# Kernel optimization log

Hardware: AMD Instinct MI355X
Metric: run time of the kernel (lower is better)

## Reference

```python
import jax, jax.numpy as jnp
import numpy as np

NUM_GROUPS = 32
EPS = 1e-6


def group_norm(x, gamma, beta):
    b, c, h, w = x.shape
    xg = x.reshape(b, NUM_GROUPS, c // NUM_GROUPS, h, w)
    mean = jnp.mean(xg, axis=(2, 3, 4), keepdims=True)
    var = jnp.var(xg, axis=(2, 3, 4), keepdims=True)
    xg = (xg - mean) * jax.lax.rsqrt(var + EPS)
    x = xg.reshape(b, c, h, w)
    return x * gamma[None, :, None, None] + beta[None, :, None, None]


def conv1x1(x, w, b):
    # x: [B,C,H,W], w: [Cout,Cin], b: [Cout]
    return jnp.einsum('bchw,oc->bohw', x, w) + b[None, :, None, None]


def setup_inputs() -> dict:
    key = jax.random.key(0)
    ks = jax.random.split(key, 11)
    B, C, H, W = 2, 512, 64, 64
    s = 1.0 / np.sqrt(C)
    return {
        'x': jax.random.normal(ks[0], (B, C, H, W), jnp.float32),
        'norm_gamma': jnp.ones((C,), jnp.float32),
        'norm_beta': jnp.zeros((C,), jnp.float32),
        'wq': jax.random.normal(ks[1], (C, C), jnp.float32) * s,
        'bq': jnp.zeros((C,), jnp.float32),
        'wk': jax.random.normal(ks[2], (C, C), jnp.float32) * s,
        'bk': jnp.zeros((C,), jnp.float32),
        'wv': jax.random.normal(ks[3], (C, C), jnp.float32) * s,
        'bv': jnp.zeros((C,), jnp.float32),
        'wo': jax.random.normal(ks[4], (C, C), jnp.float32) * s,
        'bo': jnp.zeros((C,), jnp.float32),
    }


def reference(x, norm_gamma, norm_beta, wq, bq, wk, bk, wv, bv, wo, bo):
    b, c, h, w = x.shape
    hn = group_norm(x, norm_gamma, norm_beta)
    q = conv1x1(hn, wq, bq).reshape(b, c, h * w)  # [B,C,HW]
    k = conv1x1(hn, wk, bk).reshape(b, c, h * w)
    v = conv1x1(hn, wv, bv).reshape(b, c, h * w)
    scale = jnp.asarray(c, x.dtype) ** -0.5
    # scores[b,i,j] = sum_c q[b,c,i] * k[b,c,j]
    scores = jnp.einsum('bci,bcj->bij', q, k) * scale
    attn = jax.nn.softmax(scores, axis=2)
    # out[b,c,i] = sum_j v[b,c,j] * attn[b,i,j]
    out = jnp.einsum('bcj,bij->bci', v, attn).reshape(b, c, h, w)
    out = conv1x1(out, wo, bo)
    return x + out
```

## Files before the change

### kernel.cpp

```cpp
#include <hip/hip_runtime.h>
#include <hip/hip_bf16.h>

using u16 = unsigned short;
typedef __attribute__((ext_vector_type(4))) float f32x4;
typedef __attribute__((ext_vector_type(8))) __bf16 bf16x8;
typedef __attribute__((ext_vector_type(8))) short s16x8;
typedef __attribute__((ext_vector_type(4))) short s16x4;

#define DEVI __device__ __forceinline__

constexpr int BATCH = 2, C = 512, HW = 4096, NG = 32, CPG = 16;

DEVI float b2f(u16 u) { union { unsigned u; float f; } a; a.u = ((unsigned)u) << 16; return a.f; }
DEVI u16 f2b(float f) {
  union { float f; unsigned u; } a; a.f = f;
  unsigned r = a.u + 0x7fffu + ((a.u >> 16) & 1u);
  return (u16)(r >> 16);
}

DEVI void xcd_remap(int& bx, int& by, int& bz) {
  const int nx = gridDim.x, ny = gridDim.y;
  const int nwg = nx * ny * gridDim.z;
  const int flat = blockIdx.x + nx * (blockIdx.y + ny * blockIdx.z);
  const int cpx = nwg >> 3;
  const int w = (flat & 7) * cpx + (flat >> 3);
  bx = w % nx;
  const int t = w / nx;
  by = t % ny;
  bz = t / ny;
}

__global__ __launch_bounds__(256) void cvt_w(const float* __restrict__ a, const float* __restrict__ b,
                                             const float* __restrict__ c, const float* __restrict__ d,
                                             u16* __restrict__ out) {
  int i = blockIdx.x * 256 + threadIdx.x;
  int w = i >> 16;
  int off = (i & 65535) * 4;
  const float* s = (w == 0) ? a : (w == 1) ? b : (w == 2) ? c : d;
  f32x4 v = *(const f32x4*)(s + off);
  s16x4 o;
  o[0] = (short)f2b(v[0]); o[1] = (short)f2b(v[1]); o[2] = (short)f2b(v[2]); o[3] = (short)f2b(v[3]);
  *(s16x4*)(out + (size_t)w * 262144 + off) = o;
}

__global__ __launch_bounds__(1024) void gn_stats(const float* __restrict__ x, float* __restrict__ stats) {
  int bg = blockIdx.x;
  const f32x4* xg = (const f32x4*)(x + (size_t)bg * (CPG * HW));
  float s = 0.f, ss = 0.f;
  for (int i = threadIdx.x; i < CPG * HW / 4; i += 1024) {
    f32x4 v = xg[i];
    s += v[0] + v[1] + v[2] + v[3];
    ss += v[0] * v[0] + v[1] * v[1] + v[2] * v[2] + v[3] * v[3];
  }
  #pragma unroll
  for (int o = 32; o; o >>= 1) { s += __shfl_xor(s, o); ss += __shfl_xor(ss, o); }
  __shared__ float red[32];
  int wv = threadIdx.x >> 6, ln = threadIdx.x & 63;
  if (ln == 0) { red[wv] = s; red[16 + wv] = ss; }
  __syncthreads();
  if (threadIdx.x == 0) {
    float S = 0.f, SS = 0.f;
    for (int i = 0; i < 16; ++i) { S += red[i]; SS += red[16 + i]; }
    float inv = 1.f / (float)(CPG * HW);
    float mean = S * inv;
    float var = SS * inv - mean * mean;
    stats[bg * 2] = mean;
    stats[bg * 2 + 1] = rsqrtf(var + 1e-6f);
  }
}

__global__ __launch_bounds__(256) void gn_normT(const float* __restrict__ x, const float* __restrict__ stats,
                                                const float* __restrict__ gamma, const float* __restrict__ beta,
                                                u16* __restrict__ hnT) {
  __shared__ u16 tile[64][66];
  int b = blockIdx.z, c0 = blockIdx.y * 64, h0 = blockIdx.x * 64;
  int t = threadIdx.x;
  const float* xb = x + ((size_t)b * C + c0) * HW + h0;
  int r = t / 16, cc = (t % 16) * 4;
  #pragma unroll
  for (int it = 0; it < 4; ++it) {
    int rr = it * 16 + r;
    int ch = c0 + rr;
    int g = b * NG + (ch >> 4);
    float mean = stats[g * 2], rstd = stats[g * 2 + 1];
    float ga = gamma[ch] * rstd;
    float be = beta[ch] - mean * ga;
    f32x4 v = *(const f32x4*)(xb + (size_t)rr * HW + cc);
    #pragma unroll
    for (int j = 0; j < 4; ++j) tile[rr][cc + j] = f2b(v[j] * ga + be);
  }
  __syncthreads();
  u16* op = hnT + (size_t)b * HW * C + (size_t)h0 * C + c0;
  int hr2 = t / 8, cg = (t % 8) * 8;
  #pragma unroll
  for (int it = 0; it < 2; ++it) {
    int hr = it * 32 + hr2;
    s16x8 o8;
    #pragma unroll
    for (int j = 0; j < 8; ++j) o8[j] = (short)tile[cg + j][hr];
    *(s16x8*)(op + (size_t)hr * C + cg) = o8;
  }
}

#define EPI_BIAS_M 1
#define EPI_BIAS_N 2
#define EPI_RESID  4
#define EPI_F32OUT 8
#define EPI_QK     32

template <int EPI>
__global__ __launch_bounds__(256) void gemm_bt(const u16* __restrict__ A, const u16* __restrict__ Bt,
                                               void* __restrict__ Co, int M, int N, int K,
                                               long long sA, long long sB, long long sC,
                                               const float* __restrict__ bias,
                                               const float* __restrict__ biasB,
                                               const float* __restrict__ resid, long long sR) {
  (void)M;
  __shared__ u16 ldsA[128 * 64];
  __shared__ u16 ldsB[128 * 64];
  const int tid = threadIdx.x;
  int bn, bm, bz;
  xcd_remap(bn, bm, bz);
  A += (size_t)bz * sA;
  Bt += (size_t)bz * sB;
  const int wave = tid >> 6, lane = tid & 63;
  const int wr = wave >> 1, wc = wave & 1;
  f32x4 acc[4][4] = {};

  const int srow = tid >> 3;
  const int sch = (tid & 7) ^ (srow & 7);
  const u16* gA = A + (size_t)(bm * 128 + srow) * K + sch * 8;
  const u16* gB = Bt + (size_t)(bn * 128 + srow) * K + sch * 8;
  u16* lA = ldsA + wave * 512;
  u16* lB = ldsB + wave * 512;

  for (int k0 = 0; k0 < K; k0 += 64) {
    #pragma unroll
    for (int cc = 0; cc < 4; ++cc) {
      __builtin_amdgcn_global_load_lds(
          (const __attribute__((address_space(1))) void*)(gA + (size_t)cc * 32 * K + k0),
          (__attribute__((address_space(3))) void*)(lA + cc * 2048), 16, 0, 0);
      __builtin_amdgcn_global_load_lds(
          (const __attribute__((address_space(1))) void*)(gB + (size_t)cc * 32 * K + k0),
          (__attribute__((address_space(3))) void*)(lB + cc * 2048), 16, 0, 0);
    }
    __syncthreads();
    #pragma unroll
    for (int kk = 0; kk < 2; ++kk) {
      bf16x8 af[4], bfv[4];
      #pragma unroll
      for (int m = 0; m < 4; ++m) {
        int r = wr * 64 + m * 16 + (lane & 15);
        int chunk = (kk * 4 + (lane >> 4)) ^ (r & 7);
        af[m] = *(const bf16x8*)(ldsA + r * 64 + chunk * 8);
      }
      #pragma unroll
      for (int n = 0; n < 4; ++n) {
        int r = wc * 64 + n * 16 + (lane & 15);
        int chunk = (kk * 4 + (lane >> 4)) ^ (r & 7);
        bfv[n] = *(const bf16x8*)(ldsB + r * 64 + chunk * 8);
      }
      #pragma unroll
      for (int m = 0; m < 4; ++m)
        #pragma unroll
        for (int n = 0; n < 4; ++n)
          acc[m][n] = __builtin_amdgcn_mfma_f32_16x16x32_bf16(af[m], bfv[n], acc[m][n], 0, 0, 0);
    }
    __syncthreads();
  }

  const int col0 = bn * 128 + wc * 64;
  const int row0 = bm * 128 + wr * 64 + ((lane >> 4) << 2);
  #pragma unroll
  for (int m = 0; m < 4; ++m) {
    #pragma unroll
    for (int j = 0; j < 4; ++j) {
      int gm = row0 + m * 16 + j;
      float bm_v = (EPI & EPI_BIAS_M) ? bias[gm] : 0.f;
      #pragma unroll
      for (int n = 0; n < 4; ++n) {
        int gn = col0 + n * 16 + (lane & 15);
        float v = acc[m][n][j] + bm_v;
        if (EPI & EPI_BIAS_N) {
          if (EPI & EPI_QK) v += (gn < 512) ? bias[gn] : biasB[gn - 512];
          else v += bias[gn];
        }
        if (EPI & EPI_RESID) v += resid[(size_t)bz * sR + (size_t)gm * N + gn];
        if (EPI & EPI_F32OUT)
          ((float*)Co)[(size_t)bz * sC + (size_t)gm * N + gn] = v;
        else
          ((u16*)Co)[(size_t)bz * sC + (size_t)gm * N + gn] = f2b(v);
      }
    }
  }
}

template <bool SCALED>
__global__ __launch_bounds__(512, 2) void gemm256(
    const u16* __restrict__ Ag, const u16* __restrict__ Bg,
    u16* __restrict__ Co, u16* __restrict__ Co2, int zSwitch,
    int Nld, int ldK, int nsplitLog, int kLen,
    long long sA, long long sB, long long sC, float scale) {
  __shared__ u16 lds[65536];
  const int tid = threadIdx.x;
  const int lane = tid & 63, w = tid >> 6;
  const int wm = w >> 2, wn = w & 3;
  const int l15 = lane & 15, l4 = lane >> 4;
  int bn, bm, z;
  xcd_remap(bn, bm, z);
  const int bz = z >> nsplitLog, kz = z & ((1 << nsplitLog) - 1);
  const int kStart = kz * kLen;
  const int NT = kLen >> 6;

  const int rStage = w * 8 + (lane >> 3);
  const int gch = (lane & 7) ^ (lane >> 3);
  const u16* gA = Ag + (size_t)bz * sA + (size_t)(bm * 256) * ldK + kStart + gch * 8;
  const u16* gB = Bg + (size_t)bz * sB + (size_t)(bn * 256) * ldK + kStart + gch * 8;

  f32x4 acc[8][4] = {};
  bf16x8 aF[4][2], bF[2][2][2];

  const int hB = wn >> 1, qB = wn & 1;
  const u16* pA0 = lds + (0 * 4 + wm) * 8192;
  const u16* pA1 = lds + (1 * 4 + wm) * 8192;
  const u16* pB0 = lds + (0 * 4 + 2 + hB) * 8192;
  const u16* pB1 = lds + (1 * 4 + 2 + hB) * 8192;

  #define STAGE(TT, DB, AB, HF) { \
    const u16* gbase = (AB) ? gB : gA; \
    u16* l0 = lds + ((DB) * 4 + (AB) * 2 + (HF)) * 8192 + w * 512; \
    _Pragma("unroll") for (int s = 0; s < 2; ++s) { \
      const u16* gp = gbase + (size_t)((HF) * 128 + s * 64 + rStage) * ldK + (TT) * 64; \
      __builtin_amdgcn_global_load_lds((const __attribute__((address_space(1))) void*)gp, \
          (__attribute__((address_space(3))) void*)(l0 + s * 4096), 16, 0, 0); } }

  #define LOAD_A(P, MH) { _Pragma("unroll") for (int j = 0; j < 4; ++j) \
    _Pragma("unroll") for (int kk = 0; kk < 2; ++kk) { \
      const int r_ = (MH) * 64 + j * 16 + l15; const int c_ = (kk * 4 + l4) ^ (r_ & 7); \
      aF[j][kk] = *(const bf16x8*)((P) + r_ * 64 + c_ * 8); } }

  #define LOAD_B(P, NH) { _Pragma("unroll") for (int j = 0; j < 2; ++j) \
    _Pragma("unroll") for (int kk = 0; kk < 2; ++kk) { \
      const int r_ = qB * 64 + (NH) * 32 + j * 16 + l15; const int c_ = (kk * 4 + l4) ^ (r_ & 7); \
      bF[NH][j][kk] = *(const bf16x8*)((P) + r_ * 64 + c_ * 8); } }

  #define MM(MH, NH) { __builtin_amdgcn_s_setprio(1); \
    _Pragma("unroll") for (int j = 0; j < 4; ++j) \
      _Pragma("unroll") for (int j2 = 0; j2 < 2; ++j2) \
        _Pragma("unroll") for (int kk = 0; kk < 2; ++kk) \
          acc[(MH) * 4 + j][(NH) * 2 + j2] = __builtin_amdgcn_mfma_f32_16x16x32_bf16( \
              aF[j][kk], bF[NH][j2][kk], acc[(MH) * 4 + j][(NH) * 2 + j2], 0, 0, 0); \
    __builtin_amdgcn_s_setprio(0); }

  #define BAR __builtin_amdgcn_s_barrier()
  #define WLG { asm volatile("s_waitcnt lgkmcnt(0)" ::: "memory"); __builtin_amdgcn_sched_barrier(0); }
  #define WV4 asm volatile("s_waitcnt vmcnt(4)" ::: "memory")
  #define WV0 asm volatile("s_waitcnt vmcnt(0)" ::: "memory")

  STAGE(0, 0, 1, 0); STAGE(0, 0, 1, 1);
  STAGE(0, 0, 0, 0); STAGE(0, 0, 0, 1);
  STAGE(1, 1, 1, 0); STAGE(1, 1, 1, 1);
  WV4; BAR;

  const int NI = NT / 2 - 1;
  for (int i = 0; i < NI; ++i) {
    const int t1 = 2 * i + 1, u0 = 2 * i + 2, u1 = 2 * i + 3;
    LOAD_A(pA0, 0); LOAD_B(pB0, 0); STAGE(t1, 1, 0, 0); BAR; WLG; MM(0, 0); BAR;
    LOAD_B(pB0, 1); STAGE(t1, 1, 0, 1); BAR; WLG; MM(0, 1); BAR;
    LOAD_A(pA0, 1); STAGE(u0, 0, 1, 0); BAR; WLG; MM(1, 1); BAR;
    STAGE(u0, 0, 1, 1); BAR; WLG; MM(1, 0); WV4; BAR;
    LOAD_A(pA1, 0); LOAD_B(pB1, 0); STAGE(u0, 0, 0, 0); BAR; WLG; MM(0, 0); BAR;
    LOAD_B(pB1, 1); STAGE(u0, 0, 0, 1); BAR; WLG; MM(0, 1); BAR;
    LOAD_A(pA1, 1); STAGE(u1, 1, 1, 0); BAR; WLG; MM(1, 1); BAR;
    STAGE(u1, 1, 1, 1); BAR; WLG; MM(1, 0); WV4; BAR;
  }
  {
    const int t1 = NT - 1;
    LOAD_A(pA0, 0); LOAD_B(pB0, 0); STAGE(t1, 1, 0, 0); BAR; WLG; MM(0, 0); BAR;
    LOAD_B(pB0, 1); STAGE(t1, 1, 0, 1); BAR; WLG; MM(0, 1); BAR;
    LOAD_A(pA0, 1); BAR; WLG; MM(1, 1); BAR;
    BAR; WLG; MM(1, 0); WV0; BAR;
    LOAD_A(pA1, 0); LOAD_B(pB1, 0); BAR; WLG; MM(0, 0); BAR;
    LOAD_B(pB1, 1); BAR; WLG; MM(0, 1); BAR;
    LOAD_A(pA1, 1); BAR; WLG; MM(1, 1); BAR;
    MM(1, 0);
  }
  #undef STAGE
  #undef LOAD_A
  #undef LOAD_B
  #undef MM
  #undef BAR
  #undef WLG
  #undef WV4
  #undef WV0

  {
    const int rloc = wm * 128 + l4 * 4;
    const int cloc = wn * 64 + l15;
    #pragma unroll
    for (int m = 0; m < 8; ++m) {
      #pragma unroll
      for (int j = 0; j < 4; ++j) {
        const int r_ = rloc + m * 16 + j;
        const int xr = ((r_ >> 2) & 3) << 5;
        #pragma unroll
        for (int n = 0; n < 4; ++n) {
          float v = acc[m][n][j];
          if (SCALED) v *= scale;
          *(u16*)((char*)lds + ((r_ * 512 + (cloc + n * 16) * 2) ^ xr)) = f2b(v);
        }
      }
    }
    __syncthreads();
    u16* outp = (z < zSwitch) ? (Co + (size_t)z * sC) : (Co2 + (size_t)(z - zSwitch) * sC);
    #pragma unroll
    for (int it = 0; it < 16; ++it) {
      const int idx = it * 512 + tid;
      const int r_ = idx >> 5, ch = idx & 31;
      const int xr = ((r_ >> 2) & 3) << 5;
      s16x8 d8 = *(const s16x8*)((const char*)lds + ((r_ * 512 + ch * 16) ^ xr));
      *(s16x8*)(outp + (size_t)(bm * 256 + r_) * Nld + bn * 256 + ch * 8) = d8;
    }
  }
}

__global__ __launch_bounds__(256) void softmax_rows(u16* __restrict__ S) {
  int row = blockIdx.x * 4 + (threadIdx.x >> 6);
  int lane = threadIdx.x & 63;
  s16x8* p = (s16x8*)(S + (size_t)row * 4096);
  float v[64];
  float m = -1e30f;
  #pragma unroll
  for (int j = 0; j < 8; ++j) {
    s16x8 raw = p[j * 64 + lane];
    #pragma unroll
    for (int e = 0; e < 8; ++e) {
      float f = b2f((u16)raw[e]);
      v[j * 8 + e] = f;
      m = fmaxf(m, f);
    }
  }
  #pragma unroll
  for (int o = 32; o; o >>= 1) m = fmaxf(m, __shfl_xor(m, o));
  float s = 0.f;
  #pragma unroll
  for (int i = 0; i < 64; ++i) { v[i] = __expf(v[i] - m); s += v[i]; }
  #pragma unroll
  for (int o = 32; o; o >>= 1) s += __shfl_xor(s, o);
  float r = 1.f / s;
  #pragma unroll
  for (int j = 0; j < 8; ++j) {
    s16x8 o8;
    #pragma unroll
    for (int e = 0; e < 8; ++e) o8[e] = (short)f2b(v[j * 8 + e] * r);
    p[j * 64 + lane] = o8;
  }
}

__global__ __launch_bounds__(256) void reduce_pv(const u16* __restrict__ P, const u16* __restrict__ P2,
                                                 u16* __restrict__ ao) {
  const size_t e = ((size_t)blockIdx.x * 256 + threadIdx.x) * 8;
  const int b = (int)(e >> 21);
  const size_t o = e & 2097151;
  float s[8] = {0.f, 0.f, 0.f, 0.f, 0.f, 0.f, 0.f, 0.f};
  #pragma unroll
  for (int kz = 0; kz < 4; ++kz) {
    const int zz = b * 4 + kz;
    const u16* src = (zz < 6) ? (P + (size_t)zz * 2097152) : (P2 + (size_t)(zz - 6) * 2097152);
    s16x8 v = *(const s16x8*)(src + o);
    #pragma unroll
    for (int j = 0; j < 8; ++j) s[j] += b2f((u16)v[j]);
  }
  s16x8 o8;
  #pragma unroll
  for (int j = 0; j < 8; ++j) o8[j] = (short)f2b(s[j]);
  *(s16x8*)(ao + e) = o8;
}

extern "C" void kernel_launch(void* const* d_in, const int* in_sizes, int n_in,
                              void* d_out, int out_size, void* d_ws, size_t ws_size,
                              hipStream_t stream) {
  (void)in_sizes; (void)n_in; (void)out_size; (void)ws_size;
  const float* x     = (const float*)d_in[0];
  const float* gamma = (const float*)d_in[1];
  const float* beta  = (const float*)d_in[2];
  const float* wq    = (const float*)d_in[3];
  const float* bq    = (const float*)d_in[4];
  const float* wk    = (const float*)d_in[5];
  const float* bk    = (const float*)d_in[6];
  const float* wv    = (const float*)d_in[7];
  const float* bv    = (const float*)d_in[8];
  const float* wo    = (const float*)d_in[9];
  const float* bo    = (const float*)d_in[10];

  char* ws = (char*)d_ws;
  const size_t MiB = 1024 * 1024;
  float* stats = (float*)ws;
  u16* wbf = (u16*)(ws + 1024);
  u16* vv  = (u16*)(ws + 4 * MiB);
  u16* qkT = (u16*)(ws + 12 * MiB);
  u16* hnT = (u16*)(ws + 28 * MiB);
  u16* Ppart = (u16*)(ws + 12 * MiB);
  u16* Sm  = (u16*)(ws + 36 * MiB);
  u16* aoT = (u16*)(ws + 36 * MiB);

  const long long sTok  = (long long)HW * C;
  const long long sTok2 = (long long)HW * 1024;
  const long long sS    = (long long)HW * HW;
  const float scale = 0.044194173824159216f;

  cvt_w<<<dim3(1024), dim3(256), 0, stream>>>(wq, wk, wv, wo, wbf);
  gn_stats<<<dim3(64), dim3(1024), 0, stream>>>(x, stats);
  gn_normT<<<dim3(HW / 64, C / 64, BATCH), dim3(256), 0, stream>>>(x, stats, gamma, beta, hnT);

  gemm_bt<EPI_BIAS_N | EPI_QK><<<dim3(8, 32, BATCH), dim3(256), 0, stream>>>(
      hnT, wbf, qkT, HW, 1024, C, sTok, 0, sTok2, bq, bk, nullptr, 0);
  gemm_bt<EPI_BIAS_M><<<dim3(32, 4, BATCH), dim3(256), 0, stream>>>(
      wbf + 2 * 262144, hnT, vv, C, HW, C, 0, sTok, sTok, bv, nullptr, nullptr, 0);

  gemm256<true><<<dim3(16, 16, BATCH), dim3(512), 0, stream>>>(
      qkT, qkT + 512, Sm, Sm, 1000, HW, 1024, 0, C, sTok2, sTok2, sS, scale);

  softmax_rows<<<dim3(2048), dim3(256), 0, stream>>>(Sm);

  gemm256<false><<<dim3(2, 16, BATCH * 4), dim3(512), 0, stream>>>(
      Sm, vv, Ppart, (u16*)d_out, 6, C, HW, 2, HW / 4, sS, sTok, (long long)2097152, 1.f);

  reduce_pv<<<dim3(2048), dim3(256), 0, stream>>>(Ppart, (const u16*)d_out, aoT);

  gemm_bt<EPI_BIAS_M | EPI_RESID | EPI_F32OUT><<<dim3(32, 4, BATCH), dim3(256), 0, stream>>>(
      wbf + 3 * 262144, aoT, d_out, C, HW, C, 0, sTok, (long long)C * HW, bo, nullptr, x, (long long)C * HW);
}
```

Before: 178.9 us.

## Add simple double-buffered schedule variant for PV GEMM and drop explicit lgkm waits

```diff
diff --git a/kernel.cpp b/kernel.cpp
--- a/kernel.cpp
+++ b/kernel.cpp
@@ -195,7 +195,7 @@
   }
 }
 
-template <bool SCALED>
+template <bool SCALED, int SCHED>
 __global__ __launch_bounds__(512, 2) void gemm256(
     const u16* __restrict__ Ag, const u16* __restrict__ Bg,
     u16* __restrict__ Co, u16* __restrict__ Co2, int zSwitch,
@@ -219,6 +219,7 @@
 
   f32x4 acc[8][4] = {};
   bf16x8 aF[4][2], bF[2][2][2];
+  bf16x8 aFB[8][2], bFB[4][2];
 
   const int hB = wn >> 1, qB = wn & 1;
   const u16* pA0 = lds + (0 * 4 + wm) * 8192;
@@ -252,48 +253,82 @@
               aF[j][kk], bF[NH][j2][kk], acc[(MH) * 4 + j][(NH) * 2 + j2], 0, 0, 0); \
     __builtin_amdgcn_s_setprio(0); }
 
+  #define READ_ALL(PA, PB) { \
+    _Pragma("unroll") for (int m = 0; m < 8; ++m) \
+      _Pragma("unroll") for (int kk = 0; kk < 2; ++kk) { \
+        const int r_ = m * 16 + l15; const int c_ = (kk * 4 + l4) ^ (r_ & 7); \
+        aFB[m][kk] = *(const bf16x8*)((PA) + r_ * 64 + c_ * 8); } \
+    _Pragma("unroll") for (int n = 0; n < 4; ++n) \
+      _Pragma("unroll") for (int kk = 0; kk < 2; ++kk) { \
+        const int r_ = qB * 64 + n * 16 + l15; const int c_ = (kk * 4 + l4) ^ (r_ & 7); \
+        bFB[n][kk] = *(const bf16x8*)((PB) + r_ * 64 + c_ * 8); } }
+
+  #define MM_ALL { __builtin_amdgcn_s_setprio(1); \
+    _Pragma("unroll") for (int m = 0; m < 8; ++m) \
+      _Pragma("unroll") for (int n = 0; n < 4; ++n) \
+        _Pragma("unroll") for (int kk = 0; kk < 2; ++kk) \
+          acc[m][n] = __builtin_amdgcn_mfma_f32_16x16x32_bf16( \
+              aFB[m][kk], bFB[n][kk], acc[m][n], 0, 0, 0); \
+    __builtin_amdgcn_s_setprio(0); }
+
   #define BAR __builtin_amdgcn_s_barrier()
-  #define WLG { asm volatile("s_waitcnt lgkmcnt(0)" ::: "memory"); __builtin_amdgcn_sched_barrier(0); }
   #define WV4 asm volatile("s_waitcnt vmcnt(4)" ::: "memory")
   #define WV0 asm volatile("s_waitcnt vmcnt(0)" ::: "memory")
 
-  STAGE(0, 0, 1, 0); STAGE(0, 0, 1, 1);
-  STAGE(0, 0, 0, 0); STAGE(0, 0, 0, 1);
-  STAGE(1, 1, 1, 0); STAGE(1, 1, 1, 1);
-  WV4; BAR;
-
-  const int NI = NT / 2 - 1;
-  for (int i = 0; i < NI; ++i) {
-    const int t1 = 2 * i + 1, u0 = 2 * i + 2, u1 = 2 * i + 3;
-    LOAD_A(pA0, 0); LOAD_B(pB0, 0); STAGE(t1, 1, 0, 0); BAR; WLG; MM(0, 0); BAR;
-    LOAD_B(pB0, 1); STAGE(t1, 1, 0, 1); BAR; WLG; MM(0, 1); BAR;
-    LOAD_A(pA0, 1); STAGE(u0, 0, 1, 0); BAR; WLG; MM(1, 1); BAR;
-    STAGE(u0, 0, 1, 1); BAR; WLG; MM(1, 0); WV4; BAR;
-    LOAD_A(pA1, 0); LOAD_B(pB1, 0); STAGE(u0, 0, 0, 0); BAR; WLG; MM(0, 0); BAR;
-    LOAD_B(pB1, 1); STAGE(u0, 0, 0, 1); BAR; WLG; MM(0, 1); BAR;
-    LOAD_A(pA1, 1); STAGE(u1, 1, 1, 0); BAR; WLG; MM(1, 1); BAR;
-    STAGE(u1, 1, 1, 1); BAR; WLG; MM(1, 0); WV4; BAR;
-  }
-  {
-    const int t1 = NT - 1;
-    LOAD_A(pA0, 0); LOAD_B(pB0, 0); STAGE(t1, 1, 0, 0); BAR; WLG; MM(0, 0); BAR;
-    LOAD_B(pB0, 1); STAGE(t1, 1, 0, 1); BAR; WLG; MM(0, 1); BAR;
-    LOAD_A(pA0, 1); BAR; WLG; MM(1, 1); BAR;
-    BAR; WLG; MM(1, 0); WV0; BAR;
-    LOAD_A(pA1, 0); LOAD_B(pB1, 0); BAR; WLG; MM(0, 0); BAR;
-    LOAD_B(pB1, 1); BAR; WLG; MM(0, 1); BAR;
-    LOAD_A(pA1, 1); BAR; WLG; MM(1, 1); BAR;
-    MM(1, 0);
+  if constexpr (SCHED == 0) {
+    STAGE(0, 0, 1, 0); STAGE(0, 0, 1, 1);
+    STAGE(0, 0, 0, 0); STAGE(0, 0, 0, 1);
+    STAGE(1, 1, 1, 0); STAGE(1, 1, 1, 1);
+    WV4; BAR;
+
+    const int NI = NT / 2 - 1;
+    for (int i = 0; i < NI; ++i) {
+      const int t1 = 2 * i + 1, u0 = 2 * i + 2, u1 = 2 * i + 3;
+      LOAD_A(pA0, 0); LOAD_B(pB0, 0); STAGE(t1, 1, 0, 0); BAR; MM(0, 0); BAR;
+      LOAD_B(pB0, 1); STAGE(t1, 1, 0, 1); BAR; MM(0, 1); BAR;
+      LOAD_A(pA0, 1); STAGE(u0, 0, 1, 0); BAR; MM(1, 1); BAR;
+      STAGE(u0, 0, 1, 1); BAR; MM(1, 0); WV4; BAR;
+      LOAD_A(pA1, 0); LOAD_B(pB1, 0); STAGE(u0, 0, 0, 0); BAR; MM(0, 0); BAR;
+      LOAD_B(pB1, 1); STAGE(u0, 0, 0, 1); BAR; MM(0, 1); BAR;
+      LOAD_A(pA1, 1); STAGE(u1, 1, 1, 0); BAR; MM(1, 1); BAR;
+      STAGE(u1, 1, 1, 1); BAR; MM(1, 0); WV4; BAR;
+    }
+    {
+      const int t1 = NT - 1;
+      LOAD_A(pA0, 0); LOAD_B(pB0, 0); STAGE(t1, 1, 0, 0); BAR; MM(0, 0); BAR;
+      LOAD_B(pB0, 1); STAGE(t1, 1, 0, 1); BAR; MM(0, 1); BAR;
+      LOAD_A(pA0, 1); BAR; MM(1, 1); BAR;
+      BAR; MM(1, 0); WV0; BAR;
+      LOAD_A(pA1, 0); LOAD_B(pB1, 0); BAR; MM(0, 0); BAR;
+      LOAD_B(pB1, 1); BAR; MM(0, 1); BAR;
+      LOAD_A(pA1, 1); BAR; MM(1, 1); BAR;
+      MM(1, 0);
+    }
+  } else {
+    STAGE(0, 0, 0, 0); STAGE(0, 0, 0, 1); STAGE(0, 0, 1, 0); STAGE(0, 0, 1, 1);
+    WV0; BAR;
+    for (int t = 0; t < NT; t += 2) {
+      if (t + 1 < NT) { STAGE(t + 1, 1, 0, 0); STAGE(t + 1, 1, 0, 1); STAGE(t + 1, 1, 1, 0); STAGE(t + 1, 1, 1, 1); }
+      READ_ALL(pA0, pB0);
+      MM_ALL;
+      WV0; BAR;
+      if (t + 2 < NT) { STAGE(t + 2, 0, 0, 0); STAGE(t + 2, 0, 0, 1); STAGE(t + 2, 0, 1, 0); STAGE(t + 2, 0, 1, 1); }
+      READ_ALL(pA1, pB1);
+      MM_ALL;
+      WV0; BAR;
+    }
   }
   #undef STAGE
   #undef LOAD_A
   #undef LOAD_B
   #undef MM
+  #undef READ_ALL
+  #undef MM_ALL
   #undef BAR
-  #undef WLG
   #undef WV4
   #undef WV0
 
+  __syncthreads();
   {
     const int rloc = wm * 128 + l4 * 4;
     const int cloc = wn * 64 + l15;
@@ -418,12 +453,12 @@
   gemm_bt<EPI_BIAS_M><<<dim3(32, 4, BATCH), dim3(256), 0, stream>>>(
       wbf + 2 * 262144, hnT, vv, C, HW, C, 0, sTok, sTok, bv, nullptr, nullptr, 0);
 
-  gemm256<true><<<dim3(16, 16, BATCH), dim3(512), 0, stream>>>(
+  gemm256<true, 0><<<dim3(16, 16, BATCH), dim3(512), 0, stream>>>(
       qkT, qkT + 512, Sm, Sm, 1000, HW, 1024, 0, C, sTok2, sTok2, sS, scale);
 
   softmax_rows<<<dim3(2048), dim3(256), 0, stream>>>(Sm);
 
-  gemm256<false><<<dim3(2, 16, BATCH * 4), dim3(512), 0, stream>>>(
+  gemm256<false, 1><<<dim3(2, 16, BATCH * 4), dim3(512), 0, stream>>>(
       Sm, vv, Ppart, (u16*)d_out, 6, C, HW, 2, HW / 4, sS, sTok, (long long)2097152, 1.f);
 
   reduce_pv<<<dim3(2048), dim3(256), 0, stream>>>(Ppart, (const u16*)d_out, aoT);
```

Result: slower. 198.6 us (+11.1%).
